# Kernel optimization log

Hardware: AMD Instinct MI355X
Metric: run time of the kernel (lower is better)

Reference implementation:

```python
import jax, jax.numpy as jnp
from jax import lax
import numpy as np

T, B, N, F, H = 256, 32, 16, 128, 256

def setup_inputs() -> dict:
    key = jax.random.key(0)
    ks = jax.random.split(key, 6)
    scale = 1.0 / np.sqrt(H)
    return {
        "x": jax.random.normal(ks[0], (T, B, N, F), dtype=jnp.float32),
        "dones": jax.random.randint(ks[1], (T, B, N), 0, 2, dtype=jnp.int32),
        "h0": jnp.zeros((B, N, H), dtype=jnp.float32),
        "W_ih": (jax.random.normal(ks[2], (3 * H, F), dtype=jnp.float32) * scale),
        "W_hh": (jax.random.normal(ks[3], (3 * H, H), dtype=jnp.float32) * scale),
        "b_ih": (jax.random.uniform(ks[4], (3 * H,), dtype=jnp.float32, minval=-scale, maxval=scale)),
        "b_hh": (jax.random.uniform(ks[5], (3 * H,), dtype=jnp.float32, minval=-scale, maxval=scale)),
    }

def reference(x, dones, h0, W_ih, W_hh, b_ih, b_hh):
    Tt, Bb, Nn, Ff = x.shape
    Hh = W_hh.shape[1]
    BN = Bb * Nn
    xf = x.reshape(Tt, BN, Ff)
    d = dones.reshape(Tt, BN, 1).astype(x.dtype)
    # Precompute input-side gate projections for all timesteps: [T, BN, 3H]
    xg = jnp.einsum("tbf,gf->tbg", xf, W_ih) + b_ih

    def step(h, inp):
        xg_t, d_t = inp
        h = h * (1.0 - d_t)  # done-mask reset before the cell
        hg = h @ W_hh.T + b_hh
        xr, xz, xn = jnp.split(xg_t, 3, axis=-1)
        hr, hz, hn = jnp.split(hg, 3, axis=-1)
        r = jax.nn.sigmoid(xr + hr)
        z = jax.nn.sigmoid(xz + hz)
        n = jnp.tanh(xn + r * hn)
        h_new = (1.0 - z) * n + z * h
        return h_new, h_new

    _, outs = lax.scan(step, h0.reshape(BN, Hh), (xg, d))
    out_seq = outs.reshape(Tt, Bb, Nn, Hh)
    final_h = out_seq[-1][None]  # [1, B, N, H]
    return out_seq, final_h
```

## Files before the change

### kernel.cpp

```cpp
#include <hip/hip_runtime.h>
#include <math.h>

#define T_   256
#define B_   32
#define N_   16
#define F_   128
#define H_   256
#define BN_  512
#define G3_  768
#define CL_  32
#define NC_  8

typedef __attribute__((ext_vector_type(8))) short  bf16x8;
typedef __attribute__((ext_vector_type(4))) float  f32x4;
typedef __attribute__((ext_vector_type(4))) unsigned short u16x4;

#define OFF_H1   0ULL
#define OFF_HIN  4194304ULL
#define OFF_WBF  8388608ULL
#define OFF_DM   8781824ULL
#define OFF_XG   8798208ULL
#define WS_NEED  210124800ULL

__device__ __forceinline__ unsigned short f2bf(float f) {
    union { float f; unsigned u; } v; v.f = f;
    unsigned u = v.u + 0x7FFFu + ((v.u >> 16) & 1u);
    return (unsigned short)(u >> 16);
}
__device__ __forceinline__ float bf2f(unsigned short h) {
    union { unsigned u; float f; } v; v.u = ((unsigned)h) << 16;
    return v.f;
}
__device__ __forceinline__ bf16x8 load_pack8(const float* __restrict__ p) {
    f32x4 a = *(const f32x4*)p;
    f32x4 b = *(const f32x4*)(p + 4);
    bf16x8 r;
    r[0]=(short)f2bf(a[0]); r[1]=(short)f2bf(a[1]); r[2]=(short)f2bf(a[2]); r[3]=(short)f2bf(a[3]);
    r[4]=(short)f2bf(b[0]); r[5]=(short)f2bf(b[1]); r[6]=(short)f2bf(b[2]); r[7]=(short)f2bf(b[3]);
    return r;
}
__device__ __forceinline__ float sigmoidf_(float x) { return 1.0f / (1.0f + __expf(-x)); }
__device__ __forceinline__ float tanhf_(float x)    { return 1.0f - 2.0f / (__expf(2.0f * x) + 1.0f); }

__device__ __forceinline__ bf16x8 pin_a(bf16x8 v) {
    bf16x8 r;
    asm("" : "=a"(r) : "0"(v));
    return r;
}

__device__ __forceinline__ size_t xg2_idx(int tt, int seq, int g) {
    return ((((size_t)tt * 32 + (seq >> 4)) * 48 + (g >> 4)) * 64
            + ((g >> 2) & 3) * 16 + (seq & 15)) * 4 + (g & 3);
}

__global__ __launch_bounds__(512, 2)
void xg3_kernel(const float* __restrict__ x, const float* __restrict__ W_ih,
                const float* __restrict__ b_ih, const float* __restrict__ b_hh,
                const float* __restrict__ W_hh, const int* __restrict__ dones,
                unsigned short* __restrict__ xg2,
                unsigned short* __restrict__ wbf, unsigned int* __restrict__ dm)
{
    const int tid = threadIdx.x;
    if (blockIdx.x >= 256) {
        const int bid2 = blockIdx.x - 256;
        if (bid2 < 96) {
            const int i4 = bid2 * 512 + tid;
            f32x4 w = ((const f32x4*)W_hh)[i4];
            u16x4 o;
            #pragma unroll
            for (int q = 0; q < 4; ++q) o[q] = f2bf(w[q]);
            ((u16x4*)wbf)[i4] = o;
        } else {
            const int u = (bid2 - 96) * 512 + tid;
            const int c = u >> 9, s = u & 511;
            unsigned m = 0;
            #pragma unroll
            for (int k = 0; k < CL_; ++k)
                m |= (dones[(c * CL_ + k) * BN_ + s] ? 1u : 0u) << k;
            dm[c * BN_ + s] = m;
        }
        return;
    }

    __shared__ __align__(16) unsigned short xls[2][128][136];

    const int wave = tid >> 6, lane = tid & 63;
    const int lr = lane & 15, lg = lane >> 4;
    const int t  = blockIdx.x;
    const int g0 = wave * 96;

    bf16x8 wf[6][4];
    #pragma unroll
    for (int gt = 0; gt < 6; ++gt)
        #pragma unroll
        for (int kt = 0; kt < 4; ++kt)
            wf[gt][kt] = load_pack8(W_ih + (size_t)(g0 + gt*16 + lr) * F_ + kt*32 + lg*8);

    float bv[6][4];
    #pragma unroll
    for (int gt = 0; gt < 6; ++gt)
        #pragma unroll
        for (int q = 0; q < 4; ++q) {
            const int g = g0 + gt*16 + lg*4 + q;
            bv[gt][q] = b_ih[g] + (g < 2*H_ ? b_hh[g] : 0.0f);
        }

    {
        f32x4 sv0[8];
        #pragma unroll
        for (int s = 0; s < 8; ++s)
            sv0[s] = ((const f32x4*)x)[(size_t)t * 16384 + s*512 + tid];
        #pragma unroll
        for (int s = 0; s < 8; ++s) {
            u16x4 o;
            #pragma unroll
            for (int q = 0; q < 4; ++q) o[q] = f2bf(sv0[s][q]);
            const int u = s*512 + tid;
            *(u16x4*)&xls[0][u >> 5][(u & 31) * 4] = o;
        }
    }
    __syncthreads();

    int buf = 0;
    #pragma unroll 1
    for (int i = 0; i < 4; ++i) {
        f32x4 sv[8];
        if (i < 3) {
            #pragma unroll
            for (int s = 0; s < 8; ++s)
                sv[s] = ((const f32x4*)x)[(size_t)t * 16384 + (i+1)*4096 + s*512 + tid];
        }

        #pragma unroll
        for (int tbt = 0; tbt < 8; ++tbt) {
            bf16x8 xf[4];
            #pragma unroll
            for (int kt = 0; kt < 4; ++kt)
                xf[kt] = *(const bf16x8*)&xls[buf][tbt*16 + lr][kt*32 + lg*8];

            f32x4 acc[6];
            #pragma unroll
            for (int gt = 0; gt < 6; ++gt) acc[gt] = (f32x4){0.f, 0.f, 0.f, 0.f};

            #pragma unroll
            for (int kt = 0; kt < 4; ++kt)
                #pragma unroll
                for (int gt = 0; gt < 6; ++gt)
                    acc[gt] = __builtin_amdgcn_mfma_f32_16x16x32_bf16(wf[gt][kt], xf[kt], acc[gt], 0, 0, 0);

            const int sbg = i*8 + tbt;
            #pragma unroll
            for (int gt = 0; gt < 6; ++gt) {
                u16x4 o;
                #pragma unroll
                for (int q = 0; q < 4; ++q) o[q] = f2bf(acc[gt][q] + bv[gt][q]);
                const size_t base = (((size_t)t * 32 + sbg) * 48 + (wave*6 + gt)) * 64 + lane;
                *(u16x4*)(xg2 + base * 4) = o;
            }
        }

        if (i < 3) {
            #pragma unroll
            for (int s = 0; s < 8; ++s) {
                u16x4 o;
                #pragma unroll
                for (int q = 0; q < 4; ++q) o[q] = f2bf(sv[s][q]);
                const int u = s*512 + tid;
                *(u16x4*)&xls[buf ^ 1][u >> 5][(u & 31) * 4] = o;
            }
            __syncthreads();
        }
        buf ^= 1;
    }
}

__global__ __launch_bounds__(256, 1)
void pass1_kernel(const unsigned short* __restrict__ xg2,
                  const unsigned int*  __restrict__ dm,
                  const unsigned short* __restrict__ wbf,
                  const float* __restrict__ b_hh,
                  float* __restrict__ h1)
{
    __shared__ __align__(16) unsigned short hT[2][8][4][16][8];
    __shared__ __align__(16) float hpL[16][260];
    __shared__ float bhnL[H_];

    const int tid  = threadIdx.x;
    const int wave = tid >> 6, lane = tid & 63;
    const int lr = lane & 15, lg = lane >> 4;
    const int c   = blockIdx.x >> 5;
    const int bn0 = (blockIdx.x & 31) * 16;
    const int jb  = wave * 64;

    const unsigned m = dm[c * BN_ + bn0 + lr];
    if (__ballot(m != 0) == 0ULL) return;

    int last = m ? (31 - __builtin_clz(m)) : 31;
    #pragma unroll
    for (int w = 1; w < 16; w <<= 1) last = min(last, __shfl_xor(last, w));

    bhnL[tid] = b_hh[2*H_ + tid];
    #pragma unroll
    for (int sweep = 0; sweep < 2; ++sweep)
        ((bf16x8*)hT)[sweep * 256 + tid] = (bf16x8)(short)0;
    #pragma unroll
    for (int sweep = 0; sweep < 4; ++sweep) {
        const int u = sweep * 256 + tid, seq = u >> 6, jq = u & 63;
        *(f32x4*)&hpL[seq][jq * 4] = (f32x4){0.f, 0.f, 0.f, 0.f};
    }

    bf16x8 wfa[8][8];
    bf16x8 wfv[4][8];
    #pragma unroll
    for (int mt = 0; mt < 8; ++mt) {
        const int row = (mt >> 2) * H_ + jb + (mt & 3) * 16 + lr;
        #pragma unroll
        for (int kt = 0; kt < 8; ++kt)
            wfa[mt][kt] = pin_a(*(const bf16x8*)(wbf + (size_t)row * H_ + kt*32 + lg*8));
    }
    #pragma unroll
    for (int ms = 0; ms < 4; ++ms) {
        const int row = 2 * H_ + jb + ms * 16 + lr;
        #pragma unroll
        for (int kt = 0; kt < 8; ++kt)
            wfv[ms][kt] = *(const bf16x8*)(wbf + (size_t)row * H_ + kt*32 + lg*8);
    }
    __syncthreads();

    const int sb = bn0 >> 4;
    int buf = 0;
    for (int t = last; t < CL_; ++t) {
        const int tt = c * CL_ + t;
        const int tb = (tt * 32 + sb) * 48;

        u16x4 xv[3][4];
        #pragma unroll
        for (int g = 0; g < 3; ++g)
            #pragma unroll
            for (int ms = 0; ms < 4; ++ms)
                xv[g][ms] = ((const u16x4*)xg2)[(size_t)(tb + g*16 + wave*4 + ms) * 64 + lane];

        const int d = (m >> t) & 1;
        const short dms = (short)(d ? 0 : -1);

        f32x4 acc[12];
        #pragma unroll
        for (int mt = 0; mt < 8; ++mt) acc[mt] = (f32x4){0.f, 0.f, 0.f, 0.f};
        #pragma unroll
        for (int ms = 0; ms < 4; ++ms)
            acc[8 + ms] = *(const f32x4*)&bhnL[jb + ms*16 + lg*4];

        #pragma unroll
        for (int kt = 0; kt < 8; ++kt) {
            bf16x8 hv = *(const bf16x8*)&hT[buf][kt][lg][lr][0];
            hv = hv & dms;
            #pragma unroll
            for (int mt = 0; mt < 8; ++mt)
                acc[mt] = __builtin_amdgcn_mfma_f32_16x16x32_bf16(wfa[mt][kt], hv, acc[mt], 0, 0, 0);
            #pragma unroll
            for (int ms = 0; ms < 4; ++ms)
                acc[8 + ms] = __builtin_amdgcn_mfma_f32_16x16x32_bf16(wfv[ms][kt], hv, acc[8 + ms], 0, 0, 0);
        }

        #pragma unroll
        for (int ms = 0; ms < 4; ++ms) {
            const int jq = jb + ms*16 + lg*4;
            f32x4 hp4 = *(const f32x4*)&hpL[lr][jq];
            f32x4 hnew4; u16x4 hb;
            #pragma unroll
            for (int q = 0; q < 4; ++q) {
                float r = sigmoidf_(acc[0 + ms][q] + bf2f(xv[0][ms][q]));
                float z = sigmoidf_(acc[4 + ms][q] + bf2f(xv[1][ms][q]));
                float n = tanhf_(bf2f(xv[2][ms][q]) + r * acc[8 + ms][q]);
                float hpv = d ? 0.0f : hp4[q];
                float hn2 = n + z * (hpv - n);
                hnew4[q] = hn2; hb[q] = f2bf(hn2);
            }
            *(f32x4*)&hpL[lr][jq] = hnew4;
            *(u16x4*)&hT[buf ^ 1][jq >> 5][(jq >> 3) & 3][lr][jq & 7] = hb;
        }
        __syncthreads();
        buf ^= 1;
    }

    #pragma unroll
    for (int ms = 0; ms < 4; ++ms) {
        const int jq = jb + ms*16 + lg*4;
        f32x4 hv = *(const f32x4*)&hpL[lr][jq];
        *(f32x4*)(h1 + ((size_t)c * BN_ + bn0 + lr) * H_ + jq) = hv;
    }
}

__global__ __launch_bounds__(256)
void pass2_kernel(const unsigned short* __restrict__ xg2,
                  const unsigned int*  __restrict__ dm,
                  const unsigned short* __restrict__ wbf,
                  const float* __restrict__ b_hh,
                  const float* __restrict__ h0,
                  const float* __restrict__ h1,
                  float* __restrict__ hin)
{
    __shared__ unsigned short hsb[H_];
    const int s = blockIdx.x, j = threadIdx.x;
    float h = h0[(size_t)s * H_ + j];
    const float bhn = b_hh[2*H_ + j];

    for (int c = 0; c < NC_; ++c) {
        hin[((size_t)c * BN_ + s) * H_ + j] = h;
        if (c == NC_ - 1) break;
        const unsigned m = dm[c * BN_ + s];
        if (m) {
            h = h1[((size_t)c * BN_ + s) * H_ + j];
        } else {
            for (int t = 0; t < CL_; ++t) {
                hsb[j] = f2bf(h);
                __syncthreads();
                float a0 = 0.f, a1 = 0.f, a2 = 0.f;
                for (int k = 0; k < H_; ++k) {
                    float hk = bf2f(hsb[k]);
                    a0 = fmaf(bf2f(wbf[(size_t)j * H_ + k]),          hk, a0);
                    a1 = fmaf(bf2f(wbf[(size_t)(H_ + j) * H_ + k]),   hk, a1);
                    a2 = fmaf(bf2f(wbf[(size_t)(2*H_ + j) * H_ + k]), hk, a2);
                }
                const int tt = c * CL_ + t;
                float xr = bf2f(xg2[xg2_idx(tt, s, j)]);
                float xz = bf2f(xg2[xg2_idx(tt, s, H_ + j)]);
                float xn = bf2f(xg2[xg2_idx(tt, s, 2*H_ + j)]);
                float r = sigmoidf_(a0 + xr);
                float z = sigmoidf_(a1 + xz);
                float n = tanhf_(xn + r * (a2 + bhn));
                h = n + z * (h - n);
                __syncthreads();
            }
        }
    }
}

__global__ __launch_bounds__(256, 1)
void pass3_kernel(const unsigned short* __restrict__ xg2,
                  const unsigned int*  __restrict__ dm,
                  const unsigned short* __restrict__ wbf,
                  const float* __restrict__ b_hh,
                  const float* __restrict__ hin,
                  float* __restrict__ out)
{
    __shared__ __align__(16) unsigned short hT[2][8][4][16][8];
    __shared__ __align__(16) float hpL[16][260];
    __shared__ float bhnL[H_];

    const int tid  = threadIdx.x;
    const int wave = tid >> 6, lane = tid & 63;
    const int lr = lane & 15, lg = lane >> 4;
    const int c   = blockIdx.x >> 5;
    const int bn0 = (blockIdx.x & 31) * 16;
    const int jb  = wave * 64;

    const unsigned m = dm[c * BN_ + bn0 + lr];

    bhnL[tid] = b_hh[2*H_ + tid];
    #pragma unroll
    for (int sweep = 0; sweep < 4; ++sweep) {
        const int u = sweep * 256 + tid, seq = u >> 6, jq = u & 63;
        f32x4 hv = ((const f32x4*)hin)[((size_t)c * BN_ + bn0 + seq) * 64 + jq];
        *(f32x4*)&hpL[seq][jq * 4] = hv;
    }
    #pragma unroll
    for (int sweep = 0; sweep < 2; ++sweep) {
        const int u = sweep * 256 + tid, col = u & 15, kb = (u >> 4) * 8;
        bf16x8 hv = load_pack8(hin + ((size_t)c * BN_ + bn0 + col) * H_ + kb);
        ((bf16x8*)hT)[u] = hv;
    }

    bf16x8 wfa[8][8];
    bf16x8 wfv[4][8];
    #pragma unroll
    for (int mt = 0; mt < 8; ++mt) {
        const int row = (mt >> 2) * H_ + jb + (mt & 3) * 16 + lr;
        #pragma unroll
        for (int kt = 0; kt < 8; ++kt)
            wfa[mt][kt] = pin_a(*(const bf16x8*)(wbf + (size_t)row * H_ + kt*32 + lg*8));
    }
    #pragma unroll
    for (int ms = 0; ms < 4; ++ms) {
        const int row = 2 * H_ + jb + ms * 16 + lr;
        #pragma unroll
        for (int kt = 0; kt < 8; ++kt)
            wfv[ms][kt] = *(const bf16x8*)(wbf + (size_t)row * H_ + kt*32 + lg*8);
    }
    __syncthreads();

    const int sb = bn0 >> 4;
    int buf = 0;
    for (int t = 0; t < CL_; ++t) {
        const int tt = c * CL_ + t;
        const int tb = (tt * 32 + sb) * 48;

        u16x4 xv[3][4];
        #pragma unroll
        for (int g = 0; g < 3; ++g)
            #pragma unroll
            for (int ms = 0; ms < 4; ++ms)
                xv[g][ms] = ((const u16x4*)xg2)[(size_t)(tb + g*16 + wave*4 + ms) * 64 + lane];

        const int d = (m >> t) & 1;
        const short dms = (short)(d ? 0 : -1);

        f32x4 acc[12];
        #pragma unroll
        for (int mt = 0; mt < 8; ++mt) acc[mt] = (f32x4){0.f, 0.f, 0.f, 0.f};
        #pragma unroll
        for (int ms = 0; ms < 4; ++ms)
            acc[8 + ms] = *(const f32x4*)&bhnL[jb + ms*16 + lg*4];

        #pragma unroll
        for (int kt = 0; kt < 8; ++kt) {
            bf16x8 hv = *(const bf16x8*)&hT[buf][kt][lg][lr][0];
            hv = hv & dms;
            #pragma unroll
            for (int mt = 0; mt < 8; ++mt)
                acc[mt] = __builtin_amdgcn_mfma_f32_16x16x32_bf16(wfa[mt][kt], hv, acc[mt], 0, 0, 0);
            #pragma unroll
            for (int ms = 0; ms < 4; ++ms)
                acc[8 + ms] = __builtin_amdgcn_mfma_f32_16x16x32_bf16(wfv[ms][kt], hv, acc[8 + ms], 0, 0, 0);
        }

        #pragma unroll
        for (int ms = 0; ms < 4; ++ms) {
            const int jq = jb + ms*16 + lg*4;
            f32x4 hp4 = *(const f32x4*)&hpL[lr][jq];
            f32x4 hnew4; u16x4 hb;
            #pragma unroll
            for (int q = 0; q < 4; ++q) {
                float r = sigmoidf_(acc[0 + ms][q] + bf2f(xv[0][ms][q]));
                float z = sigmoidf_(acc[4 + ms][q] + bf2f(xv[1][ms][q]));
                float n = tanhf_(bf2f(xv[2][ms][q]) + r * acc[8 + ms][q]);
                float hpv = d ? 0.0f : hp4[q];
                float hn2 = n + z * (hpv - n);
                hnew4[q] = hn2; hb[q] = f2bf(hn2);
            }
            *(f32x4*)&hpL[lr][jq] = hnew4;
            *(u16x4*)&hT[buf ^ 1][jq >> 5][(jq >> 3) & 3][lr][jq & 7] = hb;
            *(f32x4*)(out + ((size_t)tt * BN_ + bn0 + lr) * H_ + jq) = hnew4;
        }
        __syncthreads();
        buf ^= 1;
    }

    if (c == NC_ - 1) {
        #pragma unroll
        for (int ms = 0; ms < 4; ++ms) {
            const int jq = jb + ms*16 + lg*4;
            f32x4 hv = *(const f32x4*)&hpL[lr][jq];
            *(f32x4*)(out + (size_t)T_ * BN_ * H_ + (size_t)(bn0 + lr) * H_ + jq) = hv;
        }
    }
}

#define SPB 4
__global__ __launch_bounds__(256, 1)
void slotgru_fallback(const float* __restrict__ x, const int* __restrict__ dones,
                      const float* __restrict__ h0, const float* __restrict__ W_ih,
                      const float* __restrict__ W_hh, const float* __restrict__ b_ih,
                      const float* __restrict__ b_hh, float* __restrict__ out)
{
    __shared__ __align__(16) float xs[SPB][F_];
    __shared__ __align__(16) float hs[SPB][H_];
    const int j = threadIdx.x, bn0 = blockIdx.x * SPB;
    const float bi0 = b_ih[j], bi1 = b_ih[H_ + j], bi2 = b_ih[2*H_ + j];
    const float bh0 = b_hh[j], bh1 = b_hh[H_ + j], bh2 = b_hh[2*H_ + j];
    const float4* wi0 = (const float4*)(W_ih + (size_t)j * F_);
    const float4* wi1 = (const float4*)(W_ih + (size_t)(H_ + j) * F_);
    const float4* wi2 = (const float4*)(W_ih + (size_t)(2*H_ + j) * F_);
    const float4* wh0 = (const float4*)(W_hh + (size_t)j * H_);
    const float4* wh1 = (const float4*)(W_hh + (size_t)(H_ + j) * H_);
    const float4* wh2 = (const float4*)(W_hh + (size_t)(2*H_ + j) * H_);
    float hreg[SPB];
    #pragma unroll
    for (int s = 0; s < SPB; ++s) { float h = h0[(size_t)(bn0+s)*H_ + j]; hreg[s]=h; hs[s][j]=h; }
    for (int t = 0; t < T_; ++t) {
        int d[SPB];
        #pragma unroll
        for (int s = 0; s < SPB; ++s) d[s] = dones[(size_t)t*BN_ + bn0 + s];
        const float* xsrc = x + (size_t)((size_t)t*BN_ + bn0) * F_;
        ((float*)xs)[j] = xsrc[j]; ((float*)xs)[j+256] = xsrc[j+256];
        #pragma unroll
        for (int s = 0; s < SPB; ++s) if (d[s]) hs[s][j] = 0.0f;
        __syncthreads();
        float ax0[SPB]={0,0,0,0}, ax1[SPB]={0,0,0,0}, ax2[SPB]={0,0,0,0};
        #pragma unroll 8
        for (int cc = 0; cc < F_/4; ++cc) {
            float4 w0=wi0[cc], w1=wi1[cc], w2=wi2[cc];
            #pragma unroll
            for (int s = 0; s < SPB; ++s) {
                float4 xv = ((const float4*)xs[s])[cc];
                ax0[s]=fmaf(w0.x,xv.x,fmaf(w0.y,xv.y,fmaf(w0.z,xv.z,fmaf(w0.w,xv.w,ax0[s]))));
                ax1[s]=fmaf(w1.x,xv.x,fmaf(w1.y,xv.y,fmaf(w1.z,xv.z,fmaf(w1.w,xv.w,ax1[s]))));
                ax2[s]=fmaf(w2.x,xv.x,fmaf(w2.y,xv.y,fmaf(w2.z,xv.z,fmaf(w2.w,xv.w,ax2[s]))));
            }
        }
        float ah0[SPB]={0,0,0,0}, ah1[SPB]={0,0,0,0}, ah2[SPB]={0,0,0,0};
        if (!(d[0]&&d[1]&&d[2]&&d[3])) {
            #pragma unroll 4
            for (int cc = 0; cc < H_/4; ++cc) {
                float4 w0=wh0[cc], w1=wh1[cc], w2=wh2[cc];
                #pragma unroll
                for (int s = 0; s < SPB; ++s) if (!d[s]) {
                    float4 hv = ((const float4*)hs[s])[cc];
                    ah0[s]=fmaf(w0.x,hv.x,fmaf(w0.y,hv.y,fmaf(w0.z,hv.z,fmaf(w0.w,hv.w,ah0[s]))));
                    ah1[s]=fmaf(w1.x,hv.x,fmaf(w1.y,hv.y,fmaf(w1.z,hv.z,fmaf(w1.w,hv.w,ah1[s]))));
                    ah2[s]=fmaf(w2.x,hv.x,fmaf(w2.y,hv.y,fmaf(w2.z,hv.z,fmaf(w2.w,hv.w,ah2[s]))));
                }
            }
        }
        float hnew[SPB];
        #pragma unroll
        for (int s = 0; s < SPB; ++s) {
            float hpv = d[s] ? 0.0f : hreg[s];
            float r = sigmoidf_(ax0[s] + bi0 + ah0[s] + bh0);
            float z = sigmoidf_(ax1[s] + bi1 + ah1[s] + bh1);
            float n = tanhf_(ax2[s] + bi2 + r * (ah2[s] + bh2));
            hnew[s] = (1.0f - z) * n + z * hpv;
        }
        __syncthreads();
        #pragma unroll
        for (int s = 0; s < SPB; ++s) {
            hs[s][j] = hnew[s]; hreg[s] = hnew[s];
            out[(size_t)((size_t)t*BN_ + bn0 + s) * H_ + j] = hnew[s];
        }
    }
    #pragma unroll
    for (int s = 0; s < SPB; ++s)
        out[(size_t)T_*BN_*H_ + (size_t)(bn0+s)*H_ + j] = hreg[s];
}

extern "C" void kernel_launch(void* const* d_in, const int* in_sizes, int n_in,
                              void* d_out, int out_size, void* d_ws, size_t ws_size,
                              hipStream_t stream) {
    const float* x     = (const float*)d_in[0];
    const int*   dones = (const int*)  d_in[1];
    const float* h0    = (const float*)d_in[2];
    const float* W_ih  = (const float*)d_in[3];
    const float* W_hh  = (const float*)d_in[4];
    const float* b_ih  = (const float*)d_in[5];
    const float* b_hh  = (const float*)d_in[6];
    float*       out   = (float*)d_out;

    if (ws_size >= WS_NEED) {
        char* ws = (char*)d_ws;
        float*          h1  = (float*)(ws + OFF_H1);
        float*          hin = (float*)(ws + OFF_HIN);
        unsigned short* wbf = (unsigned short*)(ws + OFF_WBF);
        unsigned int*   dmm = (unsigned int*)(ws + OFF_DM);
        unsigned short* xg2 = (unsigned short*)(ws + OFF_XG);

        hipLaunchKernelGGL(xg3_kernel, dim3(256 + 104), dim3(512), 0, stream,
                           x, W_ih, b_ih, b_hh, W_hh, dones, xg2, wbf, dmm);
        hipLaunchKernelGGL(pass1_kernel, dim3((NC_ - 1) * 32), dim3(256), 0, stream,
                           xg2, dmm, wbf, b_hh, h1);
        hipLaunchKernelGGL(pass2_kernel, dim3(BN_), dim3(256), 0, stream,
                           xg2, dmm, wbf, b_hh, h0, h1, hin);
        hipLaunchKernelGGL(pass3_kernel, dim3(NC_ * 32), dim3(256), 0, stream,
                           xg2, dmm, wbf, b_hh, hin, out);
    } else {
        hipLaunchKernelGGL(slotgru_fallback, dim3(BN_ / SPB), dim3(256), 0, stream,
                           x, dones, h0, W_ih, W_hh, b_ih, b_hh, out);
    }
}
```

Before: 311.2 us.

## Halve chunk length and interleave two independent chunks per block

Splits the time axis into 16 chunks of 16 steps instead of 8 chunks of 32. Each block in pass1 and pass3 now advances two independent chunks together, sharing the register-resident weights and one barrier per step. The aim is to shorten the serial dependency chain per block and hide MFMA and memory latency by interleaving two independent recurrences. In exchange it doubles LDS state per block, enlarges the workspace, and makes the pass2 carry-propagation chain longer because there are more chunks.

```diff
diff --git a/kernel.cpp b/kernel.cpp
--- a/kernel.cpp
+++ b/kernel.cpp
@@ -8,19 +8,19 @@
 #define H_   256
 #define BN_  512
 #define G3_  768
-#define CL_  32
-#define NC_  8
+#define CL_  16
+#define NC_  16
 
 typedef __attribute__((ext_vector_type(8))) short  bf16x8;
 typedef __attribute__((ext_vector_type(4))) float  f32x4;
 typedef __attribute__((ext_vector_type(4))) unsigned short u16x4;
 
 #define OFF_H1   0ULL
-#define OFF_HIN  4194304ULL
-#define OFF_WBF  8388608ULL
-#define OFF_DM   8781824ULL
-#define OFF_XG   8798208ULL
-#define WS_NEED  210124800ULL
+#define OFF_HIN  8388608ULL
+#define OFF_WBF  16777216ULL
+#define OFF_DM   17170432ULL
+#define OFF_XG   17203200ULL
+#define WS_NEED  218529792ULL
 
 __device__ __forceinline__ unsigned short f2bf(float f) {
     union { float f; unsigned u; } v; v.f = f;
@@ -51,6 +51,70 @@
 __device__ __forceinline__ size_t xg2_idx(int tt, int seq, int g) {
     return ((((size_t)tt * 32 + (seq >> 4)) * 48 + (g >> 4)) * 64
             + ((g >> 2) & 3) * 16 + (seq & 15)) * 4 + (g & 3);
+}
+
+template<bool WRITE_OUT>
+__device__ __forceinline__ void gru_step_phase(
+    int t, int cc, unsigned mm, int buf,
+    int wave, int lane, int lr, int lg, int jb, int sb, int bn0,
+    unsigned short (&hTc)[2][8][4][16][8],
+    float (&hpc)[16][260],
+    const float* bhnL,
+    const bf16x8 (&wfa)[8][8], const bf16x8 (&wfv)[4][8],
+    const unsigned short* __restrict__ xg2,
+    float* __restrict__ out)
+{
+    const int tt = cc * CL_ + t;
+    const int tb = (tt * 32 + sb) * 48;
+
+    u16x4 xv[3][4];
+    #pragma unroll
+    for (int g = 0; g < 3; ++g)
+        #pragma unroll
+        for (int ms = 0; ms < 4; ++ms)
+            xv[g][ms] = ((const u16x4*)xg2)[(size_t)(tb + g*16 + wave*4 + ms) * 64 + lane];
+
+    const int d = (mm >> t) & 1;
+    const short dms = (short)(d ? 0 : -1);
+
+    f32x4 acc[12];
+    #pragma unroll
+    for (int mt = 0; mt < 8; ++mt) acc[mt] = (f32x4){0.f, 0.f, 0.f, 0.f};
+    #pragma unroll
+    for (int ms = 0; ms < 4; ++ms)
+        acc[8 + ms] = *(const f32x4*)&bhnL[jb + ms*16 + lg*4];
+
+    #pragma unroll
+    for (int kt = 0; kt < 8; ++kt) {
+        bf16x8 hv = *(const bf16x8*)&hTc[buf][kt][lg][lr][0];
+        hv = hv & dms;
+        #pragma unroll
+        for (int mt = 0; mt < 8; ++mt)
+            acc[mt] = __builtin_amdgcn_mfma_f32_16x16x32_bf16(wfa[mt][kt], hv, acc[mt], 0, 0, 0);
+        #pragma unroll
+        for (int ms = 0; ms < 4; ++ms)
+            acc[8 + ms] = __builtin_amdgcn_mfma_f32_16x16x32_bf16(wfv[ms][kt], hv, acc[8 + ms], 0, 0, 0);
+    }
+
+    #pragma unroll
+    for (int ms = 0; ms < 4; ++ms) {
+        const int jq = jb + ms*16 + lg*4;
+        f32x4 hp4 = *(const f32x4*)&hpc[lr][jq];
+        f32x4 hnew4; u16x4 hb;
+        #pragma unroll
+        for (int q = 0; q < 4; ++q) {
+            float r = sigmoidf_(acc[0 + ms][q] + bf2f(xv[0][ms][q]));
+            float z = sigmoidf_(acc[4 + ms][q] + bf2f(xv[1][ms][q]));
+            float n = tanhf_(bf2f(xv[2][ms][q]) + r * acc[8 + ms][q]);
+            float hpv = d ? 0.0f : hp4[q];
+            float hn2 = n + z * (hpv - n);
+            hnew4[q] = hn2; hb[q] = f2bf(hn2);
+        }
+        *(f32x4*)&hpc[lr][jq] = hnew4;
+        *(u16x4*)&hTc[buf ^ 1][jq >> 5][(jq >> 3) & 3][lr][jq & 7] = hb;
+        if (WRITE_OUT)
+            *(f32x4*)(out + ((size_t)tt * BN_ + bn0 + lr) * H_ + jq) = hnew4;
+    }
 }
 
 __global__ __launch_bounds__(512, 2)
@@ -181,32 +245,45 @@
                   const float* __restrict__ b_hh,
                   float* __restrict__ h1)
 {
-    __shared__ __align__(16) unsigned short hT[2][8][4][16][8];
-    __shared__ __align__(16) float hpL[16][260];
+    __shared__ __align__(16) unsigned short hT[2][2][8][4][16][8];
+    __shared__ __align__(16) float hpL[2][16][260];
     __shared__ float bhnL[H_];
 
     const int tid  = threadIdx.x;
     const int wave = tid >> 6, lane = tid & 63;
     const int lr = lane & 15, lg = lane >> 4;
-    const int c   = blockIdx.x >> 5;
-    const int bn0 = (blockIdx.x & 31) * 16;
-    const int jb  = wave * 64;
-
-    const unsigned m = dm[c * BN_ + bn0 + lr];
-    if (__ballot(m != 0) == 0ULL) return;
-
-    int last = m ? (31 - __builtin_clz(m)) : 31;
-    #pragma unroll
-    for (int w = 1; w < 16; w <<= 1) last = min(last, __shfl_xor(last, w));
+    const int pair = blockIdx.x >> 5;
+    const int bn0  = (blockIdx.x & 31) * 16;
+    const int jb   = wave * 64;
+    const int cA = 2*pair, cB = 2*pair + 1;
+
+    const unsigned mA = dm[cA * BN_ + bn0 + lr];
+    bool aAct = (__ballot(mA != 0) != 0ULL);
+    unsigned mB = 0;
+    bool bAct = false;
+    if (cB < NC_ - 1) {
+        mB = dm[cB * BN_ + bn0 + lr];
+        bAct = (__ballot(mB != 0) != 0ULL);
+    }
+    if (!aAct && !bAct) return;
+
+    int lastA = mA ? (31 - __builtin_clz(mA)) : (CL_ - 1);
+    int lastB = mB ? (31 - __builtin_clz(mB)) : (CL_ - 1);
+    #pragma unroll
+    for (int w = 1; w < 16; w <<= 1) {
+        lastA = min(lastA, __shfl_xor(lastA, w));
+        lastB = min(lastB, __shfl_xor(lastB, w));
+    }
+    const int tmin = min(aAct ? lastA : CL_ - 1, bAct ? lastB : CL_ - 1);
 
     bhnL[tid] = b_hh[2*H_ + tid];
     #pragma unroll
-    for (int sweep = 0; sweep < 2; ++sweep)
-        ((bf16x8*)hT)[sweep * 256 + tid] = (bf16x8)(short)0;
-    #pragma unroll
-    for (int sweep = 0; sweep < 4; ++sweep) {
-        const int u = sweep * 256 + tid, seq = u >> 6, jq = u & 63;
-        *(f32x4*)&hpL[seq][jq * 4] = (f32x4){0.f, 0.f, 0.f, 0.f};
+    for (int u = tid; u < 2048; u += 256)
+        ((bf16x8*)hT)[u] = (bf16x8)(short)0;
+    #pragma unroll
+    for (int u = tid; u < 2048; u += 256) {
+        const int ch = u >> 10, rem = u & 1023, seq = rem >> 6, jq4 = rem & 63;
+        *(f32x4*)&hpL[ch][seq][jq4 * 4] = (f32x4){0.f, 0.f, 0.f, 0.f};
     }
 
     bf16x8 wfa[8][8];
@@ -229,65 +306,30 @@
 
     const int sb = bn0 >> 4;
     int buf = 0;
-    for (int t = last; t < CL_; ++t) {
-        const int tt = c * CL_ + t;
-        const int tb = (tt * 32 + sb) * 48;
-
-        u16x4 xv[3][4];
-        #pragma unroll
-        for (int g = 0; g < 3; ++g)
-            #pragma unroll
-            for (int ms = 0; ms < 4; ++ms)
-                xv[g][ms] = ((const u16x4*)xg2)[(size_t)(tb + g*16 + wave*4 + ms) * 64 + lane];
-
-        const int d = (m >> t) & 1;
-        const short dms = (short)(d ? 0 : -1);
-
-        f32x4 acc[12];
-        #pragma unroll
-        for (int mt = 0; mt < 8; ++mt) acc[mt] = (f32x4){0.f, 0.f, 0.f, 0.f};
-        #pragma unroll
-        for (int ms = 0; ms < 4; ++ms)
-            acc[8 + ms] = *(const f32x4*)&bhnL[jb + ms*16 + lg*4];
-
-        #pragma unroll
-        for (int kt = 0; kt < 8; ++kt) {
-            bf16x8 hv = *(const bf16x8*)&hT[buf][kt][lg][lr][0];
-            hv = hv & dms;
-            #pragma unroll
-            for (int mt = 0; mt < 8; ++mt)
-                acc[mt] = __builtin_amdgcn_mfma_f32_16x16x32_bf16(wfa[mt][kt], hv, acc[mt], 0, 0, 0);
-            #pragma unroll
-            for (int ms = 0; ms < 4; ++ms)
-                acc[8 + ms] = __builtin_amdgcn_mfma_f32_16x16x32_bf16(wfv[ms][kt], hv, acc[8 + ms], 0, 0, 0);
-        }
-
+    for (int t = tmin; t < CL_; ++t) {
+        if (aAct && t >= lastA)
+            gru_step_phase<false>(t, cA, mA, buf, wave, lane, lr, lg, jb, sb, bn0,
+                                  hT[0], hpL[0], bhnL, wfa, wfv, xg2, (float*)0);
+        if (bAct && t >= lastB)
+            gru_step_phase<false>(t, cB, mB, buf, wave, lane, lr, lg, jb, sb, bn0,
+                                  hT[1], hpL[1], bhnL, wfa, wfv, xg2, (float*)0);
+        __syncthreads();
+        buf ^= 1;
+    }
+
+    if (aAct) {
         #pragma unroll
         for (int ms = 0; ms < 4; ++ms) {
             const int jq = jb + ms*16 + lg*4;
-            f32x4 hp4 = *(const f32x4*)&hpL[lr][jq];
-            f32x4 hnew4; u16x4 hb;
-            #pragma unroll
-            for (int q = 0; q < 4; ++q) {
-                float r = sigmoidf_(acc[0 + ms][q] + bf2f(xv[0][ms][q]));
-                float z = sigmoidf_(acc[4 + ms][q] + bf2f(xv[1][ms][q]));
-                float n = tanhf_(bf2f(xv[2][ms][q]) + r * acc[8 + ms][q]);
-                float hpv = d ? 0.0f : hp4[q];
-                float hn2 = n + z * (hpv - n);
-                hnew4[q] = hn2; hb[q] = f2bf(hn2);
-            }
-            *(f32x4*)&hpL[lr][jq] = hnew4;
-            *(u16x4*)&hT[buf ^ 1][jq >> 5][(jq >> 3) & 3][lr][jq & 7] = hb;
-        }
-        __syncthreads();
-        buf ^= 1;
-    }
-
-    #pragma unroll
-    for (int ms = 0; ms < 4; ++ms) {
-        const int jq = jb + ms*16 + lg*4;
-        f32x4 hv = *(const f32x4*)&hpL[lr][jq];
-        *(f32x4*)(h1 + ((size_t)c * BN_ + bn0 + lr) * H_ + jq) = hv;
+            *(f32x4*)(h1 + ((size_t)cA * BN_ + bn0 + lr) * H_ + jq) = *(const f32x4*)&hpL[0][lr][jq];
+        }
+    }
+    if (bAct) {
+        #pragma unroll
+        for (int ms = 0; ms < 4; ++ms) {
+            const int jq = jb + ms*16 + lg*4;
+            *(f32x4*)(h1 + ((size_t)cB * BN_ + bn0 + lr) * H_ + jq) = *(const f32x4*)&hpL[1][lr][jq];
+        }
     }
 }
 
@@ -344,31 +386,37 @@
                   const float* __restrict__ hin,
                   float* __restrict__ out)
 {
-    __shared__ __align__(16) unsigned short hT[2][8][4][16][8];
-    __shared__ __align__(16) float hpL[16][260];
+    __shared__ __align__(16) unsigned short hT[2][2][8][4][16][8];
+    __shared__ __align__(16) float hpL[2][16][260];
     __shared__ float bhnL[H_];
 
     const int tid  = threadIdx.x;
     const int wave = tid >> 6, lane = tid & 63;
     const int lr = lane & 15, lg = lane >> 4;
-    const int c   = blockIdx.x >> 5;
-    const int bn0 = (blockIdx.x & 31) * 16;
-    const int jb  = wave * 64;
-
-    const unsigned m = dm[c * BN_ + bn0 + lr];
+    const int pair = blockIdx.x >> 5;
+    const int bn0  = (blockIdx.x & 31) * 16;
+    const int jb   = wave * 64;
+    const int cA = 2*pair, cB = 2*pair + 1;
+
+    const unsigned mA = dm[cA * BN_ + bn0 + lr];
+    const unsigned mB = dm[cB * BN_ + bn0 + lr];
 
     bhnL[tid] = b_hh[2*H_ + tid];
     #pragma unroll
-    for (int sweep = 0; sweep < 4; ++sweep) {
-        const int u = sweep * 256 + tid, seq = u >> 6, jq = u & 63;
-        f32x4 hv = ((const f32x4*)hin)[((size_t)c * BN_ + bn0 + seq) * 64 + jq];
-        *(f32x4*)&hpL[seq][jq * 4] = hv;
-    }
-    #pragma unroll
-    for (int sweep = 0; sweep < 2; ++sweep) {
-        const int u = sweep * 256 + tid, col = u & 15, kb = (u >> 4) * 8;
-        bf16x8 hv = load_pack8(hin + ((size_t)c * BN_ + bn0 + col) * H_ + kb);
-        ((bf16x8*)hT)[u] = hv;
+    for (int ch = 0; ch < 2; ++ch) {
+        const int cc = cA + ch;
+        #pragma unroll
+        for (int sweep = 0; sweep < 4; ++sweep) {
+            const int u = sweep * 256 + tid, seq = u >> 6, jq = u & 63;
+            f32x4 hv = ((const f32x4*)hin)[((size_t)cc * BN_ + bn0 + seq) * 64 + jq];
+            *(f32x4*)&hpL[ch][seq][jq * 4] = hv;
+        }
+        #pragma unroll
+        for (int sweep = 0; sweep < 2; ++sweep) {
+            const int u = sweep * 256 + tid, col = u & 15, kb = (u >> 4) * 8;
+            bf16x8 hv = load_pack8(hin + ((size_t)cc * BN_ + bn0 + col) * H_ + kb);
+            ((bf16x8*)hT)[ch * 1024 + u] = hv;
+        }
     }
 
     bf16x8 wfa[8][8];
@@ -392,66 +440,20 @@
     const int sb = bn0 >> 4;
     int buf = 0;
     for (int t = 0; t < CL_; ++t) {
-        const int tt = c * CL_ + t;
-        const int tb = (tt * 32 + sb) * 48;
-
-        u16x4 xv[3][4];
-        #pragma unroll
-        for (int g = 0; g < 3; ++g)
-            #pragma unroll
-            for (int ms = 0; ms < 4; ++ms)
-                xv[g][ms] = ((const u16x4*)xg2)[(size_t)(tb + g*16 + wave*4 + ms) * 64 + lane];
-
-        const int d = (m >> t) & 1;
-        const short dms = (short)(d ? 0 : -1);
-
-        f32x4 acc[12];
-        #pragma unroll
-        for (int mt = 0; mt < 8; ++mt) acc[mt] = (f32x4){0.f, 0.f, 0.f, 0.f};
-        #pragma unroll
-        for (int ms = 0; ms < 4; ++ms)
-            acc[8 + ms] = *(const f32x4*)&bhnL[jb + ms*16 + lg*4];
-
-        #pragma unroll
-        for (int kt = 0; kt < 8; ++kt) {
-            bf16x8 hv = *(const bf16x8*)&hT[buf][kt][lg][lr][0];
-            hv = hv & dms;
-            #pragma unroll
-            for (int mt = 0; mt < 8; ++mt)
-                acc[mt] = __builtin_amdgcn_mfma_f32_16x16x32_bf16(wfa[mt][kt], hv, acc[mt], 0, 0, 0);
-            #pragma unroll
-            for (int ms = 0; ms < 4; ++ms)
-                acc[8 + ms] = __builtin_amdgcn_mfma_f32_16x16x32_bf16(wfv[ms][kt], hv, acc[8 + ms], 0, 0, 0);
-        }
-
+        gru_step_phase<true>(t, cA, mA, buf, wave, lane, lr, lg, jb, sb, bn0,
+                             hT[0], hpL[0], bhnL, wfa, wfv, xg2, out);
+        gru_step_phase<true>(t, cB, mB, buf, wave, lane, lr, lg, jb, sb, bn0,
+                             hT[1], hpL[1], bhnL, wfa, wfv, xg2, out);
+        __syncthreads();
+        buf ^= 1;
+    }
+
+    if (cB == NC_ - 1) {
         #pragma unroll
         for (int ms = 0; ms < 4; ++ms) {
             const int jq = jb + ms*16 + lg*4;
-            f32x4 hp4 = *(const f32x4*)&hpL[lr][jq];
-            f32x4 hnew4; u16x4 hb;
-            #pragma unroll
-            for (int q = 0; q < 4; ++q) {
-                float r = sigmoidf_(acc[0 + ms][q] + bf2f(xv[0][ms][q]));
-                float z = sigmoidf_(acc[4 + ms][q] + bf2f(xv[1][ms][q]));
-                float n = tanhf_(bf2f(xv[2][ms][q]) + r * acc[8 + ms][q]);
-                float hpv = d ? 0.0f : hp4[q];
-                float hn2 = n + z * (hpv - n);
-                hnew4[q] = hn2; hb[q] = f2bf(hn2);
-            }
-            *(f32x4*)&hpL[lr][jq] = hnew4;
-            *(u16x4*)&hT[buf ^ 1][jq >> 5][(jq >> 3) & 3][lr][jq & 7] = hb;
-            *(f32x4*)(out + ((size_t)tt * BN_ + bn0 + lr) * H_ + jq) = hnew4;
-        }
-        __syncthreads();
-        buf ^= 1;
-    }
-
-    if (c == NC_ - 1) {
-        #pragma unroll
-        for (int ms = 0; ms < 4; ++ms) {
-            const int jq = jb + ms*16 + lg*4;
-            f32x4 hv = *(const f32x4*)&hpL[lr][jq];
-            *(f32x4*)(out + (size_t)T_ * BN_ * H_ + (size_t)(bn0 + lr) * H_ + jq) = hv;
+            *(f32x4*)(out + (size_t)T_ * BN_ * H_ + (size_t)(bn0 + lr) * H_ + jq)
+                = *(const f32x4*)&hpL[1][lr][jq];
         }
     }
 }
@@ -553,13 +555,13 @@
         unsigned int*   dmm = (unsigned int*)(ws + OFF_DM);
         unsigned short* xg2 = (unsigned short*)(ws + OFF_XG);
 
-        hipLaunchKernelGGL(xg3_kernel, dim3(256 + 104), dim3(512), 0, stream,
+        hipLaunchKernelGGL(xg3_kernel, dim3(256 + 112), dim3(512), 0, stream,
                            x, W_ih, b_ih, b_hh, W_hh, dones, xg2, wbf, dmm);
-        hipLaunchKernelGGL(pass1_kernel, dim3((NC_ - 1) * 32), dim3(256), 0, stream,
+        hipLaunchKernelGGL(pass1_kernel, dim3(256), dim3(256), 0, stream,
                            xg2, dmm, wbf, b_hh, h1);
         hipLaunchKernelGGL(pass2_kernel, dim3(BN_), dim3(256), 0, stream,
                            xg2, dmm, wbf, b_hh, h0, h1, hin);
-        hipLaunchKernelGGL(pass3_kernel, dim3(NC_ * 32), dim3(256), 0, stream,
+        hipLaunchKernelGGL(pass3_kernel, dim3(256), dim3(256), 0, stream,
                            xg2, dmm, wbf, b_hh, hin, out);
     } else {
         hipLaunchKernelGGL(slotgru_fallback, dim3(BN_ / SPB), dim3(256), 0, stream,
```

Result: slower. 387.0 us (+24.4%).
